# Kernel tuning notes

Hardware: AMD Instinct MI355X
Metric: run time of the kernel (lower is better)

The kernel has to match this reference:

```python
import jax, jax.numpy as jnp
import numpy as np

D_MODEL = 256
N_HEADS = 8
N_LEVELS = 3
N_POINTS = 4
HEAD_DIM = D_MODEL // N_HEADS
SPATIAL_SHAPES = [(80, 80), (40, 40), (20, 20)]
B = 16
LEN_Q = 300
N_TOTAL = sum(h * w for h, w in SPATIAL_SHAPES)  # 8400
N_LP = N_LEVELS * N_POINTS


def setup_inputs() -> dict:
    key = jax.random.key(0)
    ks = jax.random.split(key, 8)
    s = 0.02
    return {
        "query": jax.random.normal(ks[0], (B, LEN_Q, D_MODEL), jnp.float32),
        "reference_points": jax.random.uniform(ks[1], (B, LEN_Q, N_LEVELS, 2), jnp.float32),
        "input_flatten": jax.random.normal(ks[2], (B, N_TOTAL, D_MODEL), jnp.float32),
        "W_off": jax.random.normal(ks[3], (D_MODEL, N_HEADS * N_LP * 2), jnp.float32) * s,
        "b_off": jnp.zeros((N_HEADS * N_LP * 2,), jnp.float32),
        "W_attn": jax.random.normal(ks[4], (D_MODEL, N_HEADS * N_LP), jnp.float32) * s,
        "b_attn": jnp.zeros((N_HEADS * N_LP,), jnp.float32),
        "W_val": jax.random.normal(ks[5], (D_MODEL, D_MODEL), jnp.float32) * s,
        "b_val": jnp.zeros((D_MODEL,), jnp.float32),
        "W_out": jax.random.normal(ks[6], (D_MODEL, D_MODEL), jnp.float32) * s,
        "b_out": jnp.zeros((D_MODEL,), jnp.float32),
    }


def _ms_deform_core(value, sampling_locations, attention_weights):
    # value: (B, n_heads, head_dim, N_total); locations: (B, Lq, H, L, P, 2) in [0,1]
    Bq, Lq = sampling_locations.shape[0], sampling_locations.shape[1]
    BN = Bq * N_HEADS
    grids = 2.0 * sampling_locations - 1.0
    starts = np.cumsum([0] + [h * w for h, w in SPATIAL_SHAPES])
    sampled_levels = []
    for lid, (H, W) in enumerate(SPATIAL_SHAPES):
        val_l = value[..., starts[lid]:starts[lid + 1]]                    # (B,H,hd,HW)
        val_flat = val_l.reshape(BN, HEAD_DIM, H * W).transpose(0, 2, 1)   # (BN,HW,hd)
        g = grids[:, :, :, lid].transpose(0, 2, 1, 3, 4).reshape(BN, Lq, N_POINTS, 2)
        ix = ((g[..., 0] + 1.0) * W - 1.0) / 2.0
        iy = ((g[..., 1] + 1.0) * H - 1.0) / 2.0
        ix0 = jnp.floor(ix).astype(jnp.int32)
        iy0 = jnp.floor(iy).astype(jnp.int32)
        ix1 = ix0 + 1
        iy1 = iy0 + 1
        fx = (ix - ix0.astype(ix.dtype))[..., None]
        fy = (iy - iy0.astype(iy.dtype))[..., None]

        def corner(iyc, ixc):
            valid = ((ixc >= 0) & (ixc < W) & (iyc >= 0) & (iyc < H)).astype(val_flat.dtype)
            idx = (jnp.clip(iyc, 0, H - 1) * W + jnp.clip(ixc, 0, W - 1))
            idx = idx.reshape(BN, Lq * N_POINTS, 1)
            v = jnp.take_along_axis(val_flat, idx, axis=1)
            return v.reshape(BN, Lq, N_POINTS, HEAD_DIM) * valid[..., None]

        v00 = corner(iy0, ix0)
        v01 = corner(iy0, ix1)
        v10 = corner(iy1, ix0)
        v11 = corner(iy1, ix1)
        sampled = ((1 - fx) * (1 - fy)) * v00 + (fx * (1 - fy)) * v01 \
                + ((1 - fx) * fy) * v10 + (fx * fy) * v11
        sampled_levels.append(sampled.transpose(0, 3, 1, 2))               # (BN,hd,Lq,P)
    sv = jnp.stack(sampled_levels, axis=-2).reshape(BN, HEAD_DIM, Lq, N_LP)
    a = attention_weights.transpose(0, 2, 1, 3).reshape(BN, 1, Lq, N_LP)
    out = jnp.sum(sv * a, axis=-1)                                         # (BN,hd,Lq)
    return out.reshape(Bq, D_MODEL, Lq).transpose(0, 2, 1)                 # (B,Lq,D)


def reference(query, reference_points, input_flatten,
              W_off, b_off, W_attn, b_attn, W_val, b_val, W_out, b_out):
    Bq, Lq = query.shape[0], query.shape[1]
    value = input_flatten @ W_val + b_val
    value = value.reshape(Bq, -1, N_HEADS, HEAD_DIM).transpose(0, 2, 3, 1)  # (B,H,hd,N)
    off = (query @ W_off + b_off).reshape(Bq, Lq, N_HEADS, N_LEVELS, N_POINTS, 2)
    attn = jax.nn.softmax((query @ W_attn + b_attn).reshape(Bq, Lq, N_HEADS, N_LP), axis=-1)
    # offset normalizer is (W,H) per level (x first)
    norm = jnp.array([[w, h] for h, w in SPATIAL_SHAPES], jnp.float32)
    loc = reference_points[:, :, None, :, None, :] + off / norm[None, None, None, :, None, :]
    out = _ms_deform_core(value, loc, attn)
    return out @ W_out + b_out
```

## Files before the change

### kernel.cpp

```cpp
#include <hip/hip_runtime.h>
#include <hip/hip_bf16.h>

#define DM 256
#define NH 8
#define HD 32
#define NLV 3
#define NPT 4
#define NLP 12
#define BB 16
#define LQ 300
#define NT 8400
#define MROWS (BB * NT)
#define QROWS (BB * LQ)
#define KP3 264
#define VB (MROWS / 64)

typedef __bf16 bf16x8 __attribute__((ext_vector_type(8)));
typedef float  f32x16 __attribute__((ext_vector_type(16)));

#define GPTR(x) ((const __attribute__((address_space(1))) unsigned int*)(x))
#define LPTR(x) ((__attribute__((address_space(3))) unsigned int*)(x))

__global__ void k_wt(const float* __restrict__ W_val,
                     const float* __restrict__ W_off,
                     const float* __restrict__ W_attn,
                     const float* __restrict__ W_out,
                     __hip_bfloat16* __restrict__ Wf,
                     __hip_bfloat16* __restrict__ Wf2,
                     __hip_bfloat16* __restrict__ Wf3)
{
    const int n = blockIdx.x;
    const int k = threadIdx.x;
    if (n < 256) {
        Wf[(size_t)(k >> 3) * 2048 + n * 8 + (k & 7)] =
            __float2bfloat16(W_val[(size_t)k * 256 + n]);
    } else if (n < 544) {
        const int n2 = n - 256;
        float v = (n2 < 192) ? W_off[(size_t)k * 192 + n2]
                             : W_attn[(size_t)k * 96 + (n2 - 192)];
        Wf2[(size_t)(k >> 3) * 2304 + n2 * 8 + (k & 7)] = __float2bfloat16(v);
    } else {
        const int n3 = n - 544;
        Wf3[(size_t)(k >> 3) * 2048 + n3 * 8 + (k & 7)] =
            __float2bfloat16(W_out[(size_t)k * 256 + n3]);
    }
}

__global__ __launch_bounds__(256) void k_mm1(
    const float* __restrict__ A,
    const __hip_bfloat16* __restrict__ Wf,
    const float* __restrict__ bval,
    __hip_bfloat16* __restrict__ V,
    const float* __restrict__ Q,
    const __hip_bfloat16* __restrict__ Wf2,
    const float* __restrict__ boff,
    const float* __restrict__ battn,
    float* __restrict__ off_out,
    float* __restrict__ attn_out)
{
    __shared__ __align__(16) float Asf[8192];

    const int t    = threadIdx.x;
    const int wave = t >> 6;
    const int lane = t & 63;
    const int lm   = lane & 31;
    const int kh   = lane >> 5;

    if (blockIdx.x < VB) {
        const int m0 = blockIdx.x * 64;

        f32x16 acc[2][2];
#pragma unroll
        for (int i = 0; i < 2; i++)
#pragma unroll
            for (int j = 0; j < 2; j++)
#pragma unroll
                for (int e = 0; e < 16; e++) acc[i][j][e] = 0.f;

        const __hip_bfloat16* wf0 = Wf + (size_t)(wave * 64 + lm) * 8 + kh * 2048;
        const int sw = lm & 15;

#pragma unroll
        for (int p = 0; p < 4; ++p) {
            const int row = p * 16 + (t >> 4);
            const int sc  = (t & 15) ^ (row & 15);
            const float* gsrc = A + (size_t)(m0 + row) * 256 + sc * 4;
            __builtin_amdgcn_global_load_lds(GPTR(gsrc),
                LPTR((char*)Asf + p * 4096 + (t & 192) * 16), 16, 0, 0);
        }
        __syncthreads();

#pragma unroll
        for (int it = 0; it < 4; ++it) {
            float* cur = Asf + (it & 1) * 4096;
            if (it < 3) {
                float* nxt = Asf + ((it & 1) ^ 1) * 4096;
#pragma unroll
                for (int p = 0; p < 4; ++p) {
                    const int row = p * 16 + (t >> 4);
                    const int sc  = (t & 15) ^ (row & 15);
                    const float* gsrc = A + (size_t)(m0 + row) * 256 + (it + 1) * 64 + sc * 4;
                    __builtin_amdgcn_global_load_lds(GPTR(gsrc),
                        LPTR((char*)nxt + p * 4096 + (t & 192) * 16), 16, 0, 0);
                }
            }
#pragma unroll
            for (int g4 = 0; g4 < 4; ++g4) {
                const int g  = it * 4 + g4;
                const int s0 = g4 * 4 + kh * 2;
                float4 x0 = *(const float4*)(cur + lm * 64 + (((s0)     ^ sw) << 2));
                float4 x1 = *(const float4*)(cur + lm * 64 + (((s0 + 1) ^ sw) << 2));
                float4 y0 = *(const float4*)(cur + (32 + lm) * 64 + (((s0)     ^ sw) << 2));
                float4 y1 = *(const float4*)(cur + (32 + lm) * 64 + (((s0 + 1) ^ sw) << 2));
                union { __hip_bfloat162 h2[4]; bf16x8 v; } u0, u1;
                u0.h2[0] = __float22bfloat162_rn(make_float2(x0.x, x0.y));
                u0.h2[1] = __float22bfloat162_rn(make_float2(x0.z, x0.w));
                u0.h2[2] = __float22bfloat162_rn(make_float2(x1.x, x1.y));
                u0.h2[3] = __float22bfloat162_rn(make_float2(x1.z, x1.w));
                u1.h2[0] = __float22bfloat162_rn(make_float2(y0.x, y0.y));
                u1.h2[1] = __float22bfloat162_rn(make_float2(y0.z, y0.w));
                u1.h2[2] = __float22bfloat162_rn(make_float2(y1.x, y1.y));
                u1.h2[3] = __float22bfloat162_rn(make_float2(y1.z, y1.w));
                bf16x8 b0 = *(const bf16x8*)(wf0 + (size_t)g * 4096);
                bf16x8 b1 = *(const bf16x8*)(wf0 + (size_t)g * 4096 + 256);
                acc[0][0] = __builtin_amdgcn_mfma_f32_32x32x16_bf16(u0.v, b0, acc[0][0], 0, 0, 0);
                acc[0][1] = __builtin_amdgcn_mfma_f32_32x32x16_bf16(u0.v, b1, acc[0][1], 0, 0, 0);
                acc[1][0] = __builtin_amdgcn_mfma_f32_32x32x16_bf16(u1.v, b0, acc[1][0], 0, 0, 0);
                acc[1][1] = __builtin_amdgcn_mfma_f32_32x32x16_bf16(u1.v, b1, acc[1][1], 0, 0, 0);
            }
            if (it < 3) __syncthreads();
        }

        const int bb  = m0 / NT;
        const int bnd = (bb + 1) * NT;
#pragma unroll
        for (int i = 0; i < 2; i++) {
#pragma unroll
            for (int j = 0; j < 2; j++) {
                const int n  = wave * 64 + j * 32 + lm;
                const float bn = bval[n];
                const int h  = n >> 5;
                const int d  = n & 31;
#pragma unroll
                for (int r2 = 0; r2 < 16; r2++) {
                    int rl = (r2 & 3) + 8 * (r2 >> 2) + 4 * kh;
                    int m  = m0 + i * 32 + rl;
                    int b  = bb + ((m >= bnd) ? 1 : 0);
                    int pos = m - b * NT;
                    V[((size_t)(b * NH + h) * NT + pos) * HD + d] =
                        __float2bfloat16(acc[i][j][r2] + bn);
                }
            }
        }
    } else {
        const int m0 = (blockIdx.x - VB) * 32;

        f32x16 acc[3];
#pragma unroll
        for (int j = 0; j < 3; j++)
#pragma unroll
            for (int e = 0; e < 16; e++) acc[j][e] = 0.f;

        const __hip_bfloat16* wf0 = Wf2 + (size_t)(wave * 96 + lm) * 8 + kh * 2304;
        const int sw = lm & 15;

#pragma unroll
        for (int p = 0; p < 2; ++p) {
            const int row = p * 16 + (t >> 4);
            const int sc  = (t & 15) ^ (row & 15);
            const float* gsrc = Q + (size_t)(m0 + row) * 256 + sc * 4;
            __builtin_amdgcn_global_load_lds(GPTR(gsrc),
                LPTR((char*)Asf + p * 4096 + (t & 192) * 16), 16, 0, 0);
        }
        __syncthreads();

#pragma unroll
        for (int it = 0; it < 4; ++it) {
            float* cur = Asf + (it & 1) * 2048;
            if (it < 3) {
                float* nxt = Asf + ((it & 1) ^ 1) * 2048;
#pragma unroll
                for (int p = 0; p < 2; ++p) {
                    const int row = p * 16 + (t >> 4);
                    const int sc  = (t & 15) ^ (row & 15);
                    const float* gsrc = Q + (size_t)(m0 + row) * 256 + (it + 1) * 64 + sc * 4;
                    __builtin_amdgcn_global_load_lds(GPTR(gsrc),
                        LPTR((char*)nxt + p * 4096 + (t & 192) * 16), 16, 0, 0);
                }
            }
            if (wave < 3) {
#pragma unroll
                for (int g4 = 0; g4 < 4; ++g4) {
                    const int g  = it * 4 + g4;
                    const int s0 = g4 * 4 + kh * 2;
                    float4 x0 = *(const float4*)(cur + lm * 64 + (((s0)     ^ sw) << 2));
                    float4 x1 = *(const float4*)(cur + lm * 64 + (((s0 + 1) ^ sw) << 2));
                    union { __hip_bfloat162 h2[4]; bf16x8 v; } ua;
                    ua.h2[0] = __float22bfloat162_rn(make_float2(x0.x, x0.y));
                    ua.h2[1] = __float22bfloat162_rn(make_float2(x0.z, x0.w));
                    ua.h2[2] = __float22bfloat162_rn(make_float2(x1.x, x1.y));
                    ua.h2[3] = __float22bfloat162_rn(make_float2(x1.z, x1.w));
#pragma unroll
                    for (int j = 0; j < 3; j++) {
                        bf16x8 bf = *(const bf16x8*)(wf0 + (size_t)g * 4608 + j * 256);
                        acc[j] = __builtin_amdgcn_mfma_f32_32x32x16_bf16(ua.v, bf, acc[j], 0, 0, 0);
                    }
                }
            }
            if (it < 3) __syncthreads();
        }

        if (wave < 3) {
#pragma unroll
            for (int j = 0; j < 3; j++) {
                const int n = wave * 96 + j * 32 + lm;
                const float bias_ = (n < 192) ? boff[n] : battn[n - 192];
#pragma unroll
                for (int r2 = 0; r2 < 16; r2++) {
                    int rl = (r2 & 3) + 8 * (r2 >> 2) + 4 * kh;
                    int m  = m0 + rl;
                    float v = acc[j][r2] + bias_;
                    if (n < 192) off_out[(size_t)m * 192 + n] = v;
                    else         attn_out[(size_t)m * 96 + (n - 192)] = v;
                }
            }
        }
    }
}

#define GATHER4(D0, D1, D2, D3, IV)                    \
    D0 = *(const uint4*)(vb + (IV).x);                 \
    D1 = *(const uint4*)(vb + (IV).y);                 \
    D2 = *(const uint4*)(vb + (IV).z);                 \
    D3 = *(const uint4*)(vb + (IV).w);

#define CONSUME4(C0, C1, C2, C3, W)                                          \
    {                                                                        \
        union { uint4 v; __hip_bfloat162 h2[4]; } q0_, q1_, q2_, q3_;        \
        q0_.v = C0; q1_.v = C1; q2_.v = C2; q3_.v = C3;                      \
        _Pragma("unroll")                                                    \
        for (int k_ = 0; k_ < 4; ++k_) {                                     \
            float2 p0 = __bfloat1622float2(q0_.h2[k_]);                      \
            float2 p1 = __bfloat1622float2(q1_.h2[k_]);                      \
            float2 p2 = __bfloat1622float2(q2_.h2[k_]);                      \
            float2 p3 = __bfloat1622float2(q3_.h2[k_]);                      \
            aa[2*k_]   = fmaf((W).x, p0.x, fmaf((W).y, p1.x,                 \
                         fmaf((W).z, p2.x, fmaf((W).w, p3.x, aa[2*k_]))));   \
            aa[2*k_+1] = fmaf((W).x, p0.y, fmaf((W).y, p1.y,                 \
                         fmaf((W).z, p2.y, fmaf((W).w, p3.y, aa[2*k_+1])))); \
        }                                                                    \
    }

__global__ __launch_bounds__(256) void k_sample(
    const float* __restrict__ off_raw,
    const float* __restrict__ attn_raw,
    const float* __restrict__ refp,
    const __hip_bfloat16* __restrict__ V,
    __hip_bfloat16* __restrict__ sampled)
{
    const int t = threadIdx.x;

    const int bid  = blockIdx.x;
    const int xcd  = bid & 7;
    const int slot = bid >> 3;
    const int hi   = (slot >= 75) ? 1 : 0;
    const int b    = xcd + (hi << 3);
    const int q0   = (slot - hi * 75) * 4;
    const int bq0  = b * LQ + q0;

    __shared__ float aw[4][96];
    __shared__ float wc[4][96][4];
    __shared__ int   ic[4][96][4];

    if (t < 32) {
        const int q = t >> 3, h = t & 7;
        const float* arp = attn_raw + (size_t)(bq0 + q) * 96 + h * 12;
        float4 x0 = *(const float4*)arp;
        float4 x1 = *(const float4*)(arp + 4);
        float4 x2 = *(const float4*)(arp + 8);
        float v[12] = {x0.x, x0.y, x0.z, x0.w,
                       x1.x, x1.y, x1.z, x1.w,
                       x2.x, x2.y, x2.z, x2.w};
        float mx = -1e30f;
#pragma unroll
        for (int i = 0; i < 12; i++) mx = fmaxf(mx, v[i]);
        float s = 0.f;
#pragma unroll
        for (int i = 0; i < 12; i++) { v[i] = expf(v[i] - mx); s += v[i]; }
        float inv = 1.f / s;
#pragma unroll
        for (int i = 0; i < 12; i++) aw[q][h * 12 + i] = v[i] * inv;
    }
    __syncthreads();

#pragma unroll
    for (int i = t; i < 384; i += 256) {
        const int q  = i / 96;
        const int s  = i - q * 96;
        const int bq = bq0 + q;
        const float dims[3]  = {80.f, 40.f, 20.f};
        const int startsl[3] = {0, 6400, 8000};
        const int idiml[3]   = {80, 40, 20};
        int h = s / 12, lp = s - h * 12, l = lp >> 2, p = lp & 3;
        float2 o2 = *(const float2*)(off_raw + (size_t)bq * 192 + ((h * 3 + l) * 4 + p) * 2);
        float2 r2 = *(const float2*)(refp + (size_t)bq * 6 + l * 2);
        float D  = dims[l];
        float ix = (r2.x + o2.x / D) * D - 0.5f;
        float iy = (r2.y + o2.y / D) * D - 0.5f;
        const int Dl = idiml[l];
        const int st = startsl[l];

        float fix = floorf(ix), fiy = floorf(iy);
        int ix0 = (int)fix, iy0 = (int)fiy;
        int ix1 = ix0 + 1, iy1 = iy0 + 1;
        float fx = ix - fix, fy = iy - fiy;

        float mx0 = (ix0 >= 0 && ix0 < Dl) ? 1.f : 0.f;
        float mx1 = (ix1 >= 0 && ix1 < Dl) ? 1.f : 0.f;
        float my0 = (iy0 >= 0 && iy0 < Dl) ? 1.f : 0.f;
        float my1 = (iy1 >= 0 && iy1 < Dl) ? 1.f : 0.f;

        int cx0 = min(max(ix0, 0), Dl - 1);
        int cx1 = min(max(ix1, 0), Dl - 1);
        int cy0 = min(max(iy0, 0), Dl - 1);
        int cy1 = min(max(iy1, 0), Dl - 1);

        float a = aw[q][s];
        wc[q][s][0] = (1.f - fx) * (1.f - fy) * mx0 * my0 * a;
        wc[q][s][1] = fx * (1.f - fy) * mx1 * my0 * a;
        wc[q][s][2] = (1.f - fx) * fy * mx0 * my1 * a;
        wc[q][s][3] = fx * fy * mx1 * my1 * a;
        ic[q][s][0] = (st + cy0 * Dl + cx0) * HD;
        ic[q][s][1] = (st + cy0 * Dl + cx1) * HD;
        ic[q][s][2] = (st + cy1 * Dl + cx0) * HD;
        ic[q][s][3] = (st + cy1 * Dl + cx1) * HD;
    }
    __syncthreads();

    const int q   = t >> 6;
    const int u   = t & 63;
    const int h   = u >> 3;
    const int dg  = (u >> 1) & 3;
    const int par = u & 1;
    const int dt  = dg * 8;
    const int bq  = bq0 + q;
    const __hip_bfloat16* vb = V + (size_t)(b * NH + h) * NT * HD + dt;

    float4 wv[6];
    int4   iv[6];
#pragma unroll
    for (int g = 0; g < 6; ++g) {
        const int s = h * 12 + g * 2 + par;
        wv[g] = *(const float4*)(&wc[q][s][0]);
        iv[g] = *(const int4*)(&ic[q][s][0]);
    }

    float aa[8];
#pragma unroll
    for (int k = 0; k < 8; ++k) aa[k] = 0.f;

    uint4 A0, A1, A2, A3, A4, A5, A6, A7;
    uint4 B0, B1, B2, B3, B4, B5, B6, B7;

    GATHER4(A0, A1, A2, A3, iv[0]);
    GATHER4(A4, A5, A6, A7, iv[1]);
    GATHER4(B0, B1, B2, B3, iv[2]);
    GATHER4(B4, B5, B6, B7, iv[3]);
    CONSUME4(A0, A1, A2, A3, wv[0]);
    CONSUME4(A4, A5, A6, A7, wv[1]);
    GATHER4(A0, A1, A2, A3, iv[4]);
    GATHER4(A4, A5, A6, A7, iv[5]);
    CONSUME4(B0, B1, B2, B3, wv[2]);
    CONSUME4(B4, B5, B6, B7, wv[3]);
    CONSUME4(A0, A1, A2, A3, wv[4]);
    CONSUME4(A4, A5, A6, A7, wv[5]);

#pragma unroll
    for (int k = 0; k < 8; ++k) aa[k] += __shfl_xor(aa[k], 1, 64);

    if (par == 0) {
        union { uint4 v; __hip_bfloat162 h2[4]; } ou;
        ou.h2[0] = __float22bfloat162_rn(make_float2(aa[0], aa[1]));
        ou.h2[1] = __float22bfloat162_rn(make_float2(aa[2], aa[3]));
        ou.h2[2] = __float22bfloat162_rn(make_float2(aa[4], aa[5]));
        ou.h2[3] = __float22bfloat162_rn(make_float2(aa[6], aa[7]));
        *(uint4*)(sampled + (size_t)bq * 256 + h * 32 + dt) = ou.v;
    }
}

__global__ __launch_bounds__(256) void k_outproj(
    const __hip_bfloat16* __restrict__ A,
    const __hip_bfloat16* __restrict__ Wf3,
    const float* __restrict__ bias,
    float* __restrict__ out)
{
    __shared__ __hip_bfloat16 As[32 * KP3];

    const int t    = threadIdx.x;
    const int m0   = blockIdx.x * 32;
    const int wave = t >> 6;
    const int lane = t & 63;
    const int lm   = lane & 31;
    const int kh   = lane >> 5;
    const int lk   = kh * 8;
    const int ar   = t >> 3;
    const int ak   = (t & 7) * 8;

    const __hip_bfloat16* apg = A + (size_t)(m0 + ar) * 256 + ak;
    bf16x8 rr[4];
#pragma unroll
    for (int it = 0; it < 4; ++it)
        rr[it] = *(const bf16x8*)(apg + it * 64);
#pragma unroll
    for (int it = 0; it < 4; ++it)
        *(bf16x8*)(&As[ar * KP3 + it * 64 + ak]) = rr[it];
    __syncthreads();

    f32x16 acc[2];
#pragma unroll
    for (int j = 0; j < 2; j++)
#pragma unroll
        for (int e = 0; e < 16; e++) acc[j][e] = 0.f;

    const __hip_bfloat16* wf0 = Wf3 + (size_t)(wave * 64 + lm) * 8 + kh * 2048;

#pragma unroll
    for (int ks = 0; ks < 16; ++ks) {
        bf16x8 af = *(const bf16x8*)(&As[lm * KP3 + ks * 16 + lk]);
        bf16x8 b0 = *(const bf16x8*)(wf0 + (size_t)ks * 4096);
        bf16x8 b1 = *(const bf16x8*)(wf0 + (size_t)ks * 4096 + 256);
        acc[0] = __builtin_amdgcn_mfma_f32_32x32x16_bf16(af, b0, acc[0], 0, 0, 0);
        acc[1] = __builtin_amdgcn_mfma_f32_32x32x16_bf16(af, b1, acc[1], 0, 0, 0);
    }

#pragma unroll
    for (int j = 0; j < 2; j++) {
        const int n = wave * 64 + j * 32 + lm;
        const float bn = bias[n];
#pragma unroll
        for (int r2 = 0; r2 < 16; r2++) {
            int rl = (r2 & 3) + 8 * (r2 >> 2) + 4 * kh;
            int m  = m0 + rl;
            out[(size_t)m * 256 + n] = acc[j][r2] + bn;
        }
    }
}

extern "C" void kernel_launch(void* const* d_in, const int* in_sizes, int n_in,
                              void* d_out, int out_size, void* d_ws, size_t ws_size,
                              hipStream_t stream) {
    const float* query  = (const float*)d_in[0];
    const float* refp   = (const float*)d_in[1];
    const float* inputf = (const float*)d_in[2];
    const float* W_off  = (const float*)d_in[3];
    const float* b_off  = (const float*)d_in[4];
    const float* W_attn = (const float*)d_in[5];
    const float* b_attn = (const float*)d_in[6];
    const float* W_val  = (const float*)d_in[7];
    const float* b_val  = (const float*)d_in[8];
    const float* W_out  = (const float*)d_in[9];
    const float* b_out  = (const float*)d_in[10];
    float* out = (float*)d_out;

    char* ws = (char*)d_ws;
    __hip_bfloat16* value   = (__hip_bfloat16*)ws;
    float* off_raw          = (float*)(ws + 68812800);
    float* attn_raw         = (float*)(ws + 72499200);
    __hip_bfloat16* sampled = (__hip_bfloat16*)(ws + 74342400);
    __hip_bfloat16* Wf      = (__hip_bfloat16*)(ws + 76800000);
    __hip_bfloat16* Wf2     = (__hip_bfloat16*)(ws + 76931072);
    __hip_bfloat16* Wf3     = (__hip_bfloat16*)(ws + 77078528);

    k_wt<<<800, 256, 0, stream>>>(W_val, W_off, W_attn, W_out, Wf, Wf2, Wf3);
    k_mm1<<<VB + QROWS / 32, 256, 0, stream>>>(
        inputf, Wf, b_val, value, query, Wf2, b_off, b_attn, off_raw, attn_raw);
    k_sample<<<1200, 256, 0, stream>>>(off_raw, attn_raw, refp, value, sampled);
    k_outproj<<<QROWS / 32, 256, 0, stream>>>(sampled, Wf3, b_out, out);
}
```

Measured before the change: 263.7 us.

## Enlarge k_mm1 tiles to 128 rows with 512-thread blocks and retile query GEMM

```diff
diff --git a/kernel.cpp b/kernel.cpp
--- a/kernel.cpp
+++ b/kernel.cpp
@@ -13,7 +13,7 @@
 #define MROWS (BB * NT)
 #define QROWS (BB * LQ)
 #define KP3 264
-#define VB (MROWS / 64)
+#define VB2 (MROWS / 128)
 
 typedef __bf16 bf16x8 __attribute__((ext_vector_type(8)));
 typedef float  f32x16 __attribute__((ext_vector_type(16)));
@@ -29,24 +29,24 @@
                      __hip_bfloat16* __restrict__ Wf2,
                      __hip_bfloat16* __restrict__ Wf3)
 {
-    const int n = blockIdx.x;
-    const int k = threadIdx.x;
-    if (n < 256) {
+    const int k = blockIdx.x;
+    const int n = threadIdx.x;
+    if (n < 256)
         Wf[(size_t)(k >> 3) * 2048 + n * 8 + (k & 7)] =
             __float2bfloat16(W_val[(size_t)k * 256 + n]);
-    } else if (n < 544) {
-        const int n2 = n - 256;
-        float v = (n2 < 192) ? W_off[(size_t)k * 192 + n2]
-                             : W_attn[(size_t)k * 96 + (n2 - 192)];
-        Wf2[(size_t)(k >> 3) * 2304 + n2 * 8 + (k & 7)] = __float2bfloat16(v);
-    } else {
-        const int n3 = n - 544;
+    if (n < 288) {
+        float v = (n < 192) ? W_off[(size_t)k * 192 + n]
+                            : W_attn[(size_t)k * 96 + (n - 192)];
+        Wf2[(size_t)(k >> 3) * 2304 + n * 8 + (k & 7)] = __float2bfloat16(v);
+    }
+    if (n >= 256) {
+        const int n3 = n - 256;
         Wf3[(size_t)(k >> 3) * 2048 + n3 * 8 + (k & 7)] =
             __float2bfloat16(W_out[(size_t)k * 256 + n3]);
     }
 }
 
-__global__ __launch_bounds__(256) void k_mm1(
+__global__ __launch_bounds__(512) void k_mm1(
     const float* __restrict__ A,
     const __hip_bfloat16* __restrict__ Wf,
     const float* __restrict__ bval,
@@ -58,16 +58,21 @@
     float* __restrict__ off_out,
     float* __restrict__ attn_out)
 {
-    __shared__ __align__(16) float Asf[8192];
+    __shared__ __align__(16) float Asf[16384];
 
     const int t    = threadIdx.x;
     const int wave = t >> 6;
     const int lane = t & 63;
     const int lm   = lane & 31;
     const int kh   = lane >> 5;
-
-    if (blockIdx.x < VB) {
-        const int m0 = blockIdx.x * 64;
+    const int sw   = lm & 15;
+
+    if (blockIdx.x < VB2) {
+        const int m0 = blockIdx.x * 128;
+        const int mg = wave >> 2;
+        const int ng = wave & 3;
+        const int r0 = mg * 64 + lm;
+        const int r1 = mg * 64 + 32 + lm;
 
         f32x16 acc[2][2];
 #pragma unroll
@@ -77,41 +82,40 @@
 #pragma unroll
                 for (int e = 0; e < 16; e++) acc[i][j][e] = 0.f;
 
-        const __hip_bfloat16* wf0 = Wf + (size_t)(wave * 64 + lm) * 8 + kh * 2048;
-        const int sw = lm & 15;
+        const __hip_bfloat16* wf0 = Wf + (size_t)(ng * 64 + lm) * 8 + kh * 2048;
 
 #pragma unroll
         for (int p = 0; p < 4; ++p) {
-            const int row = p * 16 + (t >> 4);
+            const int row = p * 32 + (t >> 4);
             const int sc  = (t & 15) ^ (row & 15);
             const float* gsrc = A + (size_t)(m0 + row) * 256 + sc * 4;
             __builtin_amdgcn_global_load_lds(GPTR(gsrc),
-                LPTR((char*)Asf + p * 4096 + (t & 192) * 16), 16, 0, 0);
+                LPTR((char*)Asf + p * 8192 + (t & 448) * 16), 16, 0, 0);
         }
         __syncthreads();
 
 #pragma unroll
         for (int it = 0; it < 4; ++it) {
-            float* cur = Asf + (it & 1) * 4096;
+            float* cur = Asf + (it & 1) * 8192;
             if (it < 3) {
-                float* nxt = Asf + ((it & 1) ^ 1) * 4096;
+                char* nxt = (char*)Asf + ((it & 1) ^ 1) * 32768;
 #pragma unroll
                 for (int p = 0; p < 4; ++p) {
-                    const int row = p * 16 + (t >> 4);
+                    const int row = p * 32 + (t >> 4);
                     const int sc  = (t & 15) ^ (row & 15);
                     const float* gsrc = A + (size_t)(m0 + row) * 256 + (it + 1) * 64 + sc * 4;
                     __builtin_amdgcn_global_load_lds(GPTR(gsrc),
-                        LPTR((char*)nxt + p * 4096 + (t & 192) * 16), 16, 0, 0);
+                        LPTR(nxt + p * 8192 + (t & 448) * 16), 16, 0, 0);
                 }
             }
 #pragma unroll
             for (int g4 = 0; g4 < 4; ++g4) {
                 const int g  = it * 4 + g4;
                 const int s0 = g4 * 4 + kh * 2;
-                float4 x0 = *(const float4*)(cur + lm * 64 + (((s0)     ^ sw) << 2));
-                float4 x1 = *(const float4*)(cur + lm * 64 + (((s0 + 1) ^ sw) << 2));
-                float4 y0 = *(const float4*)(cur + (32 + lm) * 64 + (((s0)     ^ sw) << 2));
-                float4 y1 = *(const float4*)(cur + (32 + lm) * 64 + (((s0 + 1) ^ sw) << 2));
+                float4 x0 = *(const float4*)(cur + r0 * 64 + (((s0)     ^ sw) << 2));
+                float4 x1 = *(const float4*)(cur + r0 * 64 + (((s0 + 1) ^ sw) << 2));
+                float4 y0 = *(const float4*)(cur + r1 * 64 + (((s0)     ^ sw) << 2));
+                float4 y1 = *(const float4*)(cur + r1 * 64 + (((s0 + 1) ^ sw) << 2));
                 union { __hip_bfloat162 h2[4]; bf16x8 v; } u0, u1;
                 u0.h2[0] = __float22bfloat162_rn(make_float2(x0.x, x0.y));
                 u0.h2[1] = __float22bfloat162_rn(make_float2(x0.z, x0.w));
@@ -137,14 +141,14 @@
         for (int i = 0; i < 2; i++) {
 #pragma unroll
             for (int j = 0; j < 2; j++) {
-                const int n  = wave * 64 + j * 32 + lm;
+                const int n  = ng * 64 + j * 32 + lm;
                 const float bn = bval[n];
                 const int h  = n >> 5;
                 const int d  = n & 31;
 #pragma unroll
                 for (int r2 = 0; r2 < 16; r2++) {
                     int rl = (r2 & 3) + 8 * (r2 >> 2) + 4 * kh;
-                    int m  = m0 + i * 32 + rl;
+                    int m  = m0 + mg * 64 + i * 32 + rl;
                     int b  = bb + ((m >= bnd) ? 1 : 0);
                     int pos = m - b * NT;
                     V[((size_t)(b * NH + h) * NT + pos) * HD + d] =
@@ -153,73 +157,87 @@
             }
         }
     } else {
-        const int m0 = (blockIdx.x - VB) * 32;
-
-        f32x16 acc[3];
-#pragma unroll
-        for (int j = 0; j < 3; j++)
-#pragma unroll
-            for (int e = 0; e < 16; e++) acc[j][e] = 0.f;
-
-        const __hip_bfloat16* wf0 = Wf2 + (size_t)(wave * 96 + lm) * 8 + kh * 2304;
-        const int sw = lm & 15;
+        const int m0 = (blockIdx.x - VB2) * 64;
+        const int r0 = lm;
+        const int r1 = 32 + lm;
+
+        f32x16 acc[2][2];
+#pragma unroll
+        for (int i = 0; i < 2; i++)
+#pragma unroll
+            for (int j = 0; j < 2; j++)
+#pragma unroll
+                for (int e = 0; e < 16; e++) acc[i][j][e] = 0.f;
+
+        const __hip_bfloat16* wfA = Wf2 + (size_t)(wave * 32 + lm) * 8 + kh * 2304;
+        const __hip_bfloat16* wfB = Wf2 + (size_t)(256 + lm) * 8 + kh * 2304;
 
 #pragma unroll
         for (int p = 0; p < 2; ++p) {
-            const int row = p * 16 + (t >> 4);
+            const int row = p * 32 + (t >> 4);
             const int sc  = (t & 15) ^ (row & 15);
             const float* gsrc = Q + (size_t)(m0 + row) * 256 + sc * 4;
             __builtin_amdgcn_global_load_lds(GPTR(gsrc),
-                LPTR((char*)Asf + p * 4096 + (t & 192) * 16), 16, 0, 0);
+                LPTR((char*)Asf + p * 8192 + (t & 448) * 16), 16, 0, 0);
         }
         __syncthreads();
 
 #pragma unroll
         for (int it = 0; it < 4; ++it) {
-            float* cur = Asf + (it & 1) * 2048;
+            float* cur = Asf + (it & 1) * 4096;
             if (it < 3) {
-                float* nxt = Asf + ((it & 1) ^ 1) * 2048;
+                char* nxt = (char*)Asf + ((it & 1) ^ 1) * 16384;
 #pragma unroll
                 for (int p = 0; p < 2; ++p) {
-                    const int row = p * 16 + (t >> 4);
+                    const int row = p * 32 + (t >> 4);
                     const int sc  = (t & 15) ^ (row & 15);
                     const float* gsrc = Q + (size_t)(m0 + row) * 256 + (it + 1) * 64 + sc * 4;
                     __builtin_amdgcn_global_load_lds(GPTR(gsrc),
-                        LPTR((char*)nxt + p * 4096 + (t & 192) * 16), 16, 0, 0);
+                        LPTR(nxt + p * 8192 + (t & 448) * 16), 16, 0, 0);
                 }
             }
-            if (wave < 3) {
-#pragma unroll
-                for (int g4 = 0; g4 < 4; ++g4) {
-                    const int g  = it * 4 + g4;
-                    const int s0 = g4 * 4 + kh * 2;
-                    float4 x0 = *(const float4*)(cur + lm * 64 + (((s0)     ^ sw) << 2));
-                    float4 x1 = *(const float4*)(cur + lm * 64 + (((s0 + 1) ^ sw) << 2));
-                    union { __hip_bfloat162 h2[4]; bf16x8 v; } ua;
-                    ua.h2[0] = __float22bfloat162_rn(make_float2(x0.x, x0.y));
-                    ua.h2[1] = __float22bfloat162_rn(make_float2(x0.z, x0.w));
-                    ua.h2[2] = __float22bfloat162_rn(make_float2(x1.x, x1.y));
-                    ua.h2[3] = __float22bfloat162_rn(make_float2(x1.z, x1.w));
-#pragma unroll
-                    for (int j = 0; j < 3; j++) {
-                        bf16x8 bf = *(const bf16x8*)(wf0 + (size_t)g * 4608 + j * 256);
-                        acc[j] = __builtin_amdgcn_mfma_f32_32x32x16_bf16(ua.v, bf, acc[j], 0, 0, 0);
-                    }
+#pragma unroll
+            for (int g4 = 0; g4 < 4; ++g4) {
+                const int g  = it * 4 + g4;
+                const int s0 = g4 * 4 + kh * 2;
+                float4 x0 = *(const float4*)(cur + r0 * 64 + (((s0)     ^ sw) << 2));
+                float4 x1 = *(const float4*)(cur + r0 * 64 + (((s0 + 1) ^ sw) << 2));
+                float4 y0 = *(const float4*)(cur + r1 * 64 + (((s0)     ^ sw) << 2));
+                float4 y1 = *(const float4*)(cur + r1 * 64 + (((s0 + 1) ^ sw) << 2));
+                union { __hip_bfloat162 h2[4]; bf16x8 v; } u0, u1;
+                u0.h2[0] = __float22bfloat162_rn(make_float2(x0.x, x0.y));
+                u0.h2[1] = __float22bfloat162_rn(make_float2(x0.z, x0.w));
+                u0.h2[2] = __float22bfloat162_rn(make_float2(x1.x, x1.y));
+                u0.h2[3] = __float22bfloat162_rn(make_float2(x1.z, x1.w));
+                u1.h2[0] = __float22bfloat162_rn(make_float2(y0.x, y0.y));
+                u1.h2[1] = __float22bfloat162_rn(make_float2(y0.z, y0.w));
+                u1.h2[2] = __float22bfloat162_rn(make_float2(y1.x, y1.y));
+                u1.h2[3] = __float22bfloat162_rn(make_float2(y1.z, y1.w));
+                bf16x8 bA = *(const bf16x8*)(wfA + (size_t)g * 4608);
+                acc[0][0] = __builtin_amdgcn_mfma_f32_32x32x16_bf16(u0.v, bA, acc[0][0], 0, 0, 0);
+                acc[1][0] = __builtin_amdgcn_mfma_f32_32x32x16_bf16(u1.v, bA, acc[1][0], 0, 0, 0);
+                if (wave == 0) {
+                    bf16x8 bB = *(const bf16x8*)(wfB + (size_t)g * 4608);
+                    acc[0][1] = __builtin_amdgcn_mfma_f32_32x32x16_bf16(u0.v, bB, acc[0][1], 0, 0, 0);
+                    acc[1][1] = __builtin_amdgcn_mfma_f32_32x32x16_bf16(u1.v, bB, acc[1][1], 0, 0, 0);
                 }
             }
             if (it < 3) __syncthreads();
         }
 
-        if (wave < 3) {
-#pragma unroll
-            for (int j = 0; j < 3; j++) {
-                const int n = wave * 96 + j * 32 + lm;
-                const float bias_ = (n < 192) ? boff[n] : battn[n - 192];
+#pragma unroll
+        for (int slot = 0; slot < 2; ++slot) {
+            if (slot == 1 && wave != 0) break;
+            const int ti = (slot == 0) ? wave : 8;
+            const int n  = ti * 32 + lm;
+            const float bias_ = (n < 192) ? boff[n] : battn[n - 192];
+#pragma unroll
+            for (int i = 0; i < 2; i++) {
 #pragma unroll
                 for (int r2 = 0; r2 < 16; r2++) {
                     int rl = (r2 & 3) + 8 * (r2 >> 2) + 4 * kh;
-                    int m  = m0 + rl;
-                    float v = acc[j][r2] + bias_;
+                    int m  = m0 + i * 32 + rl;
+                    float v = acc[i][slot][r2] + bias_;
                     if (n < 192) off_out[(size_t)m * 192 + n] = v;
                     else         attn_out[(size_t)m * 96 + (n - 192)] = v;
                 }
@@ -471,8 +489,8 @@
     __hip_bfloat16* Wf2     = (__hip_bfloat16*)(ws + 76931072);
     __hip_bfloat16* Wf3     = (__hip_bfloat16*)(ws + 77078528);
 
-    k_wt<<<800, 256, 0, stream>>>(W_val, W_off, W_attn, W_out, Wf, Wf2, Wf3);
-    k_mm1<<<VB + QROWS / 32, 256, 0, stream>>>(
+    k_wt<<<256, 512, 0, stream>>>(W_val, W_off, W_attn, W_out, Wf, Wf2, Wf3);
+    k_mm1<<<VB2 + QROWS / 64, 512, 0, stream>>>(
         inputf, Wf, b_val, value, query, Wf2, b_off, b_attn, off_raw, attn_raw);
     k_sample<<<1200, 256, 0, stream>>>(off_raw, attn_raw, refp, value, sampled);
     k_outproj<<<QROWS / 32, 256, 0, stream>>>(sampled, Wf3, b_out, out);
```

After: 268.5 us. About the same (+1.8%).

## Stage GEMM A-tiles as bf16 in padded LDS via register loads

Applied to the files above, without the earlier changes.

```diff
diff --git a/kernel.cpp b/kernel.cpp
--- a/kernel.cpp
+++ b/kernel.cpp
@@ -12,14 +12,13 @@
 #define NT 8400
 #define MROWS (BB * NT)
 #define QROWS (BB * LQ)
+#define KP2 72
+#define KPV 136
 #define KP3 264
 #define VB (MROWS / 64)
 
 typedef __bf16 bf16x8 __attribute__((ext_vector_type(8)));
 typedef float  f32x16 __attribute__((ext_vector_type(16)));
-
-#define GPTR(x) ((const __attribute__((address_space(1))) unsigned int*)(x))
-#define LPTR(x) ((__attribute__((address_space(3))) unsigned int*)(x))
 
 __global__ void k_wt(const float* __restrict__ W_val,
                      const float* __restrict__ W_off,
@@ -29,18 +28,18 @@
                      __hip_bfloat16* __restrict__ Wf2,
                      __hip_bfloat16* __restrict__ Wf3)
 {
-    const int n = blockIdx.x;
-    const int k = threadIdx.x;
-    if (n < 256) {
+    const int k = blockIdx.x;
+    const int n = threadIdx.x;
+    if (n < 256)
         Wf[(size_t)(k >> 3) * 2048 + n * 8 + (k & 7)] =
             __float2bfloat16(W_val[(size_t)k * 256 + n]);
-    } else if (n < 544) {
-        const int n2 = n - 256;
-        float v = (n2 < 192) ? W_off[(size_t)k * 192 + n2]
-                             : W_attn[(size_t)k * 96 + (n2 - 192)];
-        Wf2[(size_t)(k >> 3) * 2304 + n2 * 8 + (k & 7)] = __float2bfloat16(v);
-    } else {
-        const int n3 = n - 544;
+    if (n < 288) {
+        float v = (n < 192) ? W_off[(size_t)k * 192 + n]
+                            : W_attn[(size_t)k * 96 + (n - 192)];
+        Wf2[(size_t)(k >> 3) * 2304 + n * 8 + (k & 7)] = __float2bfloat16(v);
+    }
+    if (n >= 256) {
+        const int n3 = n - 256;
         Wf3[(size_t)(k >> 3) * 2048 + n3 * 8 + (k & 7)] =
             __float2bfloat16(W_out[(size_t)k * 256 + n3]);
     }
@@ -58,16 +57,19 @@
     float* __restrict__ off_out,
     float* __restrict__ attn_out)
 {
-    __shared__ __align__(16) float Asf[8192];
+    __shared__ __hip_bfloat16 As[2][64 * KPV];
 
     const int t    = threadIdx.x;
     const int wave = t >> 6;
     const int lane = t & 63;
     const int lm   = lane & 31;
     const int kh   = lane >> 5;
+    const int lk   = kh * 8;
 
     if (blockIdx.x < VB) {
-        const int m0 = blockIdx.x * 64;
+        const int m0  = blockIdx.x * 64;
+        const int ar2 = t >> 2;
+        const int ak2 = (t & 3) * 32;
 
         f32x16 acc[2][2];
 #pragma unroll
@@ -78,57 +80,62 @@
                 for (int e = 0; e < 16; e++) acc[i][j][e] = 0.f;
 
         const __hip_bfloat16* wf0 = Wf + (size_t)(wave * 64 + lm) * 8 + kh * 2048;
-        const int sw = lm & 15;
-
-#pragma unroll
-        for (int p = 0; p < 4; ++p) {
-            const int row = p * 16 + (t >> 4);
-            const int sc  = (t & 15) ^ (row & 15);
-            const float* gsrc = A + (size_t)(m0 + row) * 256 + sc * 4;
-            __builtin_amdgcn_global_load_lds(GPTR(gsrc),
-                LPTR((char*)Asf + p * 4096 + (t & 192) * 16), 16, 0, 0);
+        const float* ap = A + (size_t)(m0 + ar2) * 256 + ak2;
+
+        {
+            float4 v[8];
+#pragma unroll
+            for (int c = 0; c < 8; ++c) v[c] = *(const float4*)(ap + c * 4);
+#pragma unroll
+            for (int c = 0; c < 4; ++c) {
+                union { __hip_bfloat162 h2[4]; bf16x8 b; } u;
+                u.h2[0] = __float22bfloat162_rn(make_float2(v[2*c].x,   v[2*c].y));
+                u.h2[1] = __float22bfloat162_rn(make_float2(v[2*c].z,   v[2*c].w));
+                u.h2[2] = __float22bfloat162_rn(make_float2(v[2*c+1].x, v[2*c+1].y));
+                u.h2[3] = __float22bfloat162_rn(make_float2(v[2*c+1].z, v[2*c+1].w));
+                *(bf16x8*)(&As[0][ar2 * KPV + ak2 + c * 8]) = u.b;
+            }
         }
         __syncthreads();
 
-#pragma unroll
-        for (int it = 0; it < 4; ++it) {
-            float* cur = Asf + (it & 1) * 4096;
-            if (it < 3) {
-                float* nxt = Asf + ((it & 1) ^ 1) * 4096;
-#pragma unroll
-                for (int p = 0; p < 4; ++p) {
-                    const int row = p * 16 + (t >> 4);
-                    const int sc  = (t & 15) ^ (row & 15);
-                    const float* gsrc = A + (size_t)(m0 + row) * 256 + (it + 1) * 64 + sc * 4;
-                    __builtin_amdgcn_global_load_lds(GPTR(gsrc),
-                        LPTR((char*)nxt + p * 4096 + (t & 192) * 16), 16, 0, 0);
-                }
-            }
-#pragma unroll
-            for (int g4 = 0; g4 < 4; ++g4) {
-                const int g  = it * 4 + g4;
-                const int s0 = g4 * 4 + kh * 2;
-                float4 x0 = *(const float4*)(cur + lm * 64 + (((s0)     ^ sw) << 2));
-                float4 x1 = *(const float4*)(cur + lm * 64 + (((s0 + 1) ^ sw) << 2));
-                float4 y0 = *(const float4*)(cur + (32 + lm) * 64 + (((s0)     ^ sw) << 2));
-                float4 y1 = *(const float4*)(cur + (32 + lm) * 64 + (((s0 + 1) ^ sw) << 2));
-                union { __hip_bfloat162 h2[4]; bf16x8 v; } u0, u1;
-                u0.h2[0] = __float22bfloat162_rn(make_float2(x0.x, x0.y));
-                u0.h2[1] = __float22bfloat162_rn(make_float2(x0.z, x0.w));
-                u0.h2[2] = __float22bfloat162_rn(make_float2(x1.x, x1.y));
-                u0.h2[3] = __float22bfloat162_rn(make_float2(x1.z, x1.w));
-                u1.h2[0] = __float22bfloat162_rn(make_float2(y0.x, y0.y));
-                u1.h2[1] = __float22bfloat162_rn(make_float2(y0.z, y0.w));
-                u1.h2[2] = __float22bfloat162_rn(make_float2(y1.x, y1.y));
-                u1.h2[3] = __float22bfloat162_rn(make_float2(y1.z, y1.w));
-                bf16x8 b0 = *(const bf16x8*)(wf0 + (size_t)g * 4096);
-                bf16x8 b1 = *(const bf16x8*)(wf0 + (size_t)g * 4096 + 256);
-                acc[0][0] = __builtin_amdgcn_mfma_f32_32x32x16_bf16(u0.v, b0, acc[0][0], 0, 0, 0);
-                acc[0][1] = __builtin_amdgcn_mfma_f32_32x32x16_bf16(u0.v, b1, acc[0][1], 0, 0, 0);
-                acc[1][0] = __builtin_amdgcn_mfma_f32_32x32x16_bf16(u1.v, b0, acc[1][0], 0, 0, 0);
-                acc[1][1] = __builtin_amdgcn_mfma_f32_32x32x16_bf16(u1.v, b1, acc[1][1], 0, 0, 0);
-            }
-            if (it < 3) __syncthreads();
+        float4 nv[8];
+#pragma unroll
+        for (int c = 0; c < 8; ++c) nv[c] = *(const float4*)(ap + 128 + c * 4);
+
+#pragma unroll
+        for (int ks = 0; ks < 8; ++ks) {
+            bf16x8 af0 = *(const bf16x8*)(&As[0][(lm)      * KPV + ks * 16 + lk]);
+            bf16x8 af1 = *(const bf16x8*)(&As[0][(32 + lm) * KPV + ks * 16 + lk]);
+            bf16x8 b0  = *(const bf16x8*)(wf0 + (size_t)ks * 4096);
+            bf16x8 b1  = *(const bf16x8*)(wf0 + (size_t)ks * 4096 + 256);
+            acc[0][0] = __builtin_amdgcn_mfma_f32_32x32x16_bf16(af0, b0, acc[0][0], 0, 0, 0);
+            acc[0][1] = __builtin_amdgcn_mfma_f32_32x32x16_bf16(af0, b1, acc[0][1], 0, 0, 0);
+            acc[1][0] = __builtin_amdgcn_mfma_f32_32x32x16_bf16(af1, b0, acc[1][0], 0, 0, 0);
+            acc[1][1] = __builtin_amdgcn_mfma_f32_32x32x16_bf16(af1, b1, acc[1][1], 0, 0, 0);
+        }
+
+#pragma unroll
+        for (int c = 0; c < 4; ++c) {
+            union { __hip_bfloat162 h2[4]; bf16x8 b; } u;
+            u.h2[0] = __float22bfloat162_rn(make_float2(nv[2*c].x,   nv[2*c].y));
+            u.h2[1] = __float22bfloat162_rn(make_float2(nv[2*c].z,   nv[2*c].w));
+            u.h2[2] = __float22bfloat162_rn(make_float2(nv[2*c+1].x, nv[2*c+1].y));
+            u.h2[3] = __float22bfloat162_rn(make_float2(nv[2*c+1].z, nv[2*c+1].w));
+            *(bf16x8*)(&As[1][ar2 * KPV + ak2 + c * 8]) = u.b;
+        }
+        __syncthreads();
+
+#pragma unroll
+        for (int ks = 0; ks < 8; ++ks) {
+            const int g = 8 + ks;
+            bf16x8 af0 = *(const bf16x8*)(&As[1][(lm)      * KPV + ks * 16 + lk]);
+            bf16x8 af1 = *(const bf16x8*)(&As[1][(32 + lm) * KPV + ks * 16 + lk]);
+            bf16x8 b0  = *(const bf16x8*)(wf0 + (size_t)g * 4096);
+            bf16x8 b1  = *(const bf16x8*)(wf0 + (size_t)g * 4096 + 256);
+            acc[0][0] = __builtin_amdgcn_mfma_f32_32x32x16_bf16(af0, b0, acc[0][0], 0, 0, 0);
+            acc[0][1] = __builtin_amdgcn_mfma_f32_32x32x16_bf16(af0, b1, acc[0][1], 0, 0, 0);
+            acc[1][0] = __builtin_amdgcn_mfma_f32_32x32x16_bf16(af1, b0, acc[1][0], 0, 0, 0);
+            acc[1][1] = __builtin_amdgcn_mfma_f32_32x32x16_bf16(af1, b1, acc[1][1], 0, 0, 0);
         }
 
         const int bb  = m0 / NT;
@@ -154,6 +161,8 @@
         }
     } else {
         const int m0 = (blockIdx.x - VB) * 32;
+        const int ar = t >> 3;
+        const int ak = (t & 7) * 8;
 
         f32x16 acc[3];
 #pragma unroll
@@ -162,52 +171,50 @@
             for (int e = 0; e < 16; e++) acc[j][e] = 0.f;
 
         const __hip_bfloat16* wf0 = Wf2 + (size_t)(wave * 96 + lm) * 8 + kh * 2304;
-        const int sw = lm & 15;
-
-#pragma unroll
-        for (int p = 0; p < 2; ++p) {
-            const int row = p * 16 + (t >> 4);
-            const int sc  = (t & 15) ^ (row & 15);
-            const float* gsrc = Q + (size_t)(m0 + row) * 256 + sc * 4;
-            __builtin_amdgcn_global_load_lds(GPTR(gsrc),
-                LPTR((char*)Asf + p * 4096 + (t & 192) * 16), 16, 0, 0);
+
+        {
+            const float* ap = Q + (size_t)(m0 + ar) * 256 + ak;
+            float4 a0 = *(const float4*)ap;
+            float4 a1 = *(const float4*)(ap + 4);
+            union { __hip_bfloat162 h2[4]; bf16x8 v; } ua;
+            ua.h2[0] = __float22bfloat162_rn(make_float2(a0.x, a0.y));
+            ua.h2[1] = __float22bfloat162_rn(make_float2(a0.z, a0.w));
+            ua.h2[2] = __float22bfloat162_rn(make_float2(a1.x, a1.y));
+            ua.h2[3] = __float22bfloat162_rn(make_float2(a1.z, a1.w));
+            *(bf16x8*)(&As[0][ar * KP2 + ak]) = ua.v;
         }
         __syncthreads();
 
 #pragma unroll
         for (int it = 0; it < 4; ++it) {
-            float* cur = Asf + (it & 1) * 2048;
+            const int buf = it & 1;
+            float4 na0, na1;
             if (it < 3) {
-                float* nxt = Asf + ((it & 1) ^ 1) * 2048;
-#pragma unroll
-                for (int p = 0; p < 2; ++p) {
-                    const int row = p * 16 + (t >> 4);
-                    const int sc  = (t & 15) ^ (row & 15);
-                    const float* gsrc = Q + (size_t)(m0 + row) * 256 + (it + 1) * 64 + sc * 4;
-                    __builtin_amdgcn_global_load_lds(GPTR(gsrc),
-                        LPTR((char*)nxt + p * 4096 + (t & 192) * 16), 16, 0, 0);
-                }
-            }
-            if (wave < 3) {
-#pragma unroll
-                for (int g4 = 0; g4 < 4; ++g4) {
-                    const int g  = it * 4 + g4;
-                    const int s0 = g4 * 4 + kh * 2;
-                    float4 x0 = *(const float4*)(cur + lm * 64 + (((s0)     ^ sw) << 2));
-                    float4 x1 = *(const float4*)(cur + lm * 64 + (((s0 + 1) ^ sw) << 2));
-                    union { __hip_bfloat162 h2[4]; bf16x8 v; } ua;
-                    ua.h2[0] = __float22bfloat162_rn(make_float2(x0.x, x0.y));
-                    ua.h2[1] = __float22bfloat162_rn(make_float2(x0.z, x0.w));
-                    ua.h2[2] = __float22bfloat162_rn(make_float2(x1.x, x1.y));
-                    ua.h2[3] = __float22bfloat162_rn(make_float2(x1.z, x1.w));
+                const float* ap = Q + (size_t)(m0 + ar) * 256 + (it + 1) * 64 + ak;
+                na0 = *(const float4*)ap;
+                na1 = *(const float4*)(ap + 4);
+            }
+#pragma unroll
+            for (int ks = 0; ks < 4; ++ks) {
+                const int g = it * 4 + ks;
+                bf16x8 af = *(const bf16x8*)(&As[buf][lm * KP2 + ks * 16 + lk]);
+                if (wave < 3) {
 #pragma unroll
                     for (int j = 0; j < 3; j++) {
                         bf16x8 bf = *(const bf16x8*)(wf0 + (size_t)g * 4608 + j * 256);
-                        acc[j] = __builtin_amdgcn_mfma_f32_32x32x16_bf16(ua.v, bf, acc[j], 0, 0, 0);
+                        acc[j] = __builtin_amdgcn_mfma_f32_32x32x16_bf16(af, bf, acc[j], 0, 0, 0);
                     }
                 }
             }
-            if (it < 3) __syncthreads();
+            if (it < 3) {
+                union { __hip_bfloat162 h2[4]; bf16x8 v; } ua;
+                ua.h2[0] = __float22bfloat162_rn(make_float2(na0.x, na0.y));
+                ua.h2[1] = __float22bfloat162_rn(make_float2(na0.z, na0.w));
+                ua.h2[2] = __float22bfloat162_rn(make_float2(na1.x, na1.y));
+                ua.h2[3] = __float22bfloat162_rn(make_float2(na1.z, na1.w));
+                *(bf16x8*)(&As[buf ^ 1][ar * KP2 + ak]) = ua.v;
+                __syncthreads();
+            }
         }
 
         if (wave < 3) {
@@ -471,7 +478,7 @@
     __hip_bfloat16* Wf2     = (__hip_bfloat16*)(ws + 76931072);
     __hip_bfloat16* Wf3     = (__hip_bfloat16*)(ws + 77078528);
 
-    k_wt<<<800, 256, 0, stream>>>(W_val, W_off, W_attn, W_out, Wf, Wf2, Wf3);
+    k_wt<<<256, 512, 0, stream>>>(W_val, W_off, W_attn, W_out, Wf, Wf2, Wf3);
     k_mm1<<<VB + QROWS / 32, 256, 0, stream>>>(
         inputf, Wf, b_val, value, query, Wf2, b_off, b_attn, off_raw, attn_raw);
     k_sample<<<1200, 256, 0, stream>>>(off_raw, attn_raw, refp, value, sampled);
```

After: 267.1 us. About the same (+1.3%).
